# Optimization experiments

Measured on AMD Instinct MI355X. Metric: run time of the kernel, lower is better.

The kernel has to match this reference:

```python
import jax, jax.numpy as jnp
import numpy as np

B, T, NHANDS, DKP = 8, 1024, 2, 128
DM, H, DH, DFF, V, M, L = 1024, 16, 64, 4096, 2000, 256, 2
KEPS = 1e-4  # performer feature-map epsilon


def _orth_proj(key, m, d):
    # Gaussian orthogonal random features (FAVOR+), rows rescaled to chi norms
    n_blocks = int(np.ceil(m / d))
    blocks = []
    for i in range(n_blocks):
        q, _ = jnp.linalg.qr(jax.random.normal(jax.random.fold_in(key, i), (d, d)))
        blocks.append(q.T)
    mat = jnp.concatenate(blocks, 0)[:m]
    mult = jnp.linalg.norm(jax.random.normal(jax.random.fold_in(key, 10 ** 6), (m, d)), axis=1)
    return (mat * mult[:, None]).astype(jnp.float32)


def setup_inputs() -> dict:
    key = jax.random.key(0)
    ks = iter(jax.random.split(key, 64))
    w = lambda shape, s=0.02: (jax.random.normal(next(ks), shape) * s).astype(jnp.float32)
    z = lambda *shape: jnp.zeros(shape, jnp.float32)
    o = lambda *shape: jnp.ones(shape, jnp.float32)
    return {
        'x': jax.random.normal(next(ks), (B, T, NHANDS, DKP), dtype=jnp.float32),
        'Win': w((NHANDS * DKP, DM)), 'b_in': z(DM),
        'pe': jax.random.normal(next(ks), (5000, DM), dtype=jnp.float32),
        'ln1_g': o(L, DM), 'ln1_b': z(L, DM),
        'Wq': w((L, DM, DM)), 'bq': z(L, DM),
        'Wk': w((L, DM, DM)), 'bk': z(L, DM),
        'Wv': w((L, DM, DM)), 'bv': z(L, DM),
        'Wo': w((L, DM, DM)), 'bo': z(L, DM),
        'ln2_g': o(L, DM), 'ln2_b': z(L, DM),
        'W1': w((L, DM, DFF)), 'b1': z(L, DFF),
        'W2': w((L, DFF, DM)), 'b2': z(L, DM),
        'Wc': w((DM, V)), 'bc': z(V),
        'Wconv': w((64, DM, 3)), 'bconv': z(64),
        'Waux': w((64, V + 1)), 'baux': z(V + 1),
        'proj': _orth_proj(next(ks), M, DH),
    }


def _ln(x, g, b):
    mu = jnp.mean(x, -1, keepdims=True)
    var = jnp.mean((x - mu) ** 2, -1, keepdims=True)
    return (x - mu) / jnp.sqrt(var + 1e-5) * g + b


def _feats(data, proj, is_query):
    # FAVOR+ softmax kernel features, data: (B,H,T,DH) -> (B,H,T,M)
    dn = DH ** -0.25
    ratio = M ** -0.5
    dd = jnp.einsum('bhnd,md->bhnm', data, proj) * dn
    diag = jnp.sum(data ** 2, -1, keepdims=True) * 0.5 * dn * dn
    if is_query:
        stab = jnp.max(dd, -1, keepdims=True)
    else:
        stab = jnp.max(dd, (-1, -2), keepdims=True)
    return ratio * (jnp.exp(dd - diag - jax.lax.stop_gradient(stab)) + KEPS)


def reference(x, Win, b_in, pe, ln1_g, ln1_b, Wq, bq, Wk, bk, Wv, bv, Wo, bo,
              ln2_g, ln2_b, W1, b1, W2, b2, Wc, bc, Wconv, bconv, Waux, baux, proj):
    h = x.reshape(B, T, NHANDS * DKP) @ Win + b_in
    h = h + pe[:T][None]

    def layer(h, i):
        y = _ln(h, ln1_g[i], ln1_b[i])
        q = (y @ Wq[i] + bq[i]).reshape(B, T, H, DH).transpose(0, 2, 1, 3)
        k = (y @ Wk[i] + bk[i]).reshape(B, T, H, DH).transpose(0, 2, 1, 3)
        v = (y @ Wv[i] + bv[i]).reshape(B, T, H, DH).transpose(0, 2, 1, 3)
        qp = _feats(q, proj, True)   # (B,H,T,M)
        kp = _feats(k, proj, False)
        dinv = 1.0 / jnp.einsum('bhnm,bhm->bhn', qp, kp.sum(2))
        ctx = jnp.einsum('bhnm,bhnd->bhmd', kp, v)          # (B,H,M,DH)
        o = jnp.einsum('bhnm,bhmd->bhnd', qp, ctx) * dinv[..., None]
        o = o.transpose(0, 2, 1, 3).reshape(B, T, DM) @ Wo[i] + bo[i]
        h = h + o
        y = _ln(h, ln2_g[i], ln2_b[i])
        ff = jax.nn.gelu(y @ W1[i] + b1[i], approximate=False) @ W2[i] + b2[i]
        return h + ff

    h = layer(h, 0)
    xa = h.transpose(0, 2, 1)  # (B, DM, T)
    xa = jax.lax.conv_general_dilated(xa, Wconv, (1,), 'SAME',
                                      dimension_numbers=('NCH', 'OIH', 'NCH'))
    xa = xa + bconv[None, :, None]
    aux = xa.transpose(0, 2, 1) @ Waux + baux  # (B, T, V+1)
    h = layer(h, 1)
    gloss = h @ Wc + bc  # (B, T, V)
    return (gloss, aux)
```

## Files before the change

kernel.cpp:

```cpp
#include <hip/hip_runtime.h>
#include <hip/hip_bf16.h>

typedef __attribute__((ext_vector_type(4))) float f32x4;
typedef __attribute__((ext_vector_type(8))) unsigned short u16x8;
typedef __attribute__((ext_vector_type(4))) unsigned short u16x4;
typedef __bf16 bf16x8 __attribute__((ext_vector_type(8)));

#define DEVFN static __device__ __forceinline__

constexpr int CB = 8, CT = 1024, CDM = 1024, CH = 16, CDH = 64, CDFF = 4096, CV = 2000, CM = 256;
constexpr int CNT = CB * CT;
constexpr int CQKV = 3072;
constexpr float CDN = 0.35355339059327373f;
constexpr float CRATIO = 0.0625f;
constexpr float CKEPS = 1e-4f;

DEVFN unsigned short f2bu(float x) {
  __hip_bfloat16 h = __float2bfloat16(x);
  return __builtin_bit_cast(unsigned short, h);
}
DEVFN float b2f(unsigned short u) {
  __hip_bfloat16 h = __builtin_bit_cast(__hip_bfloat16, u);
  return __bfloat162float(h);
}
DEVFN float wredsum(float s) {
#pragma unroll
  for (int ofs = 32; ofs; ofs >>= 1) s += __shfl_xor(s, ofs, 64);
  return s;
}
DEVFN float wredmax(float s) {
#pragma unroll
  for (int ofs = 32; ofs; ofs >>= 1) s = fmaxf(s, __shfl_xor(s, ofs, 64));
  return s;
}
DEVFN void gl_lds16(const void* g, void* l) {
  __builtin_amdgcn_global_load_lds(
      (const __attribute__((address_space(1))) unsigned int*)g,
      (__attribute__((address_space(3))) unsigned int*)l, 16, 0, 0);
}
DEVFN f32x4 mfma16(u16x8 a, u16x8 b, f32x4 c) {
  return __builtin_amdgcn_mfma_f32_16x16x32_bf16(
      __builtin_bit_cast(bf16x8, a), __builtin_bit_cast(bf16x8, b), c, 0, 0, 0);
}
DEVFN u16x8 lds_rd128(unsigned addr) {
  u16x8 r;
  asm volatile("ds_read_b128 %0, %1" : "=v"(r) : "v"(addr));
  return r;
}
DEVFN unsigned lds_addr(const void* p) {
  return (unsigned)(unsigned long)(const __attribute__((address_space(3))) char*)p;
}

#define EPI_BIAS 1
#define EPI_ACCUM 2
#define EPI_GELU 4
#define EPI_OUTBF 8
#define EPI_RSCALE 16
#define EPI_PE 32
#define EPI_DUP 64

template <int EPI>
__global__ __launch_bounds__(512, 4) void gemm128_k(
    const unsigned short* __restrict__ A, const unsigned short* __restrict__ Bt,
    const float* __restrict__ bias, void* __restrict__ C, void* __restrict__ aux,
    int Mr, int Nr, int Kr, int lda, int ldb, int ldc) {
  __shared__ unsigned short smA[2][128 * 64];
  __shared__ unsigned short smB[2][128 * 64];

  int tid = threadIdx.x, wv = tid >> 6, ll = tid & 63;
  int wm = wv >> 2, wn = wv & 3;
  int m0 = blockIdx.x * 128, n0 = blockIdx.y * 128;
  int fr = ll & 15, f16 = ll >> 4, fk = f16 * 8;

  const char* Ab = (const char*)A;
  const char* Bb = (const char*)Bt;

  unsigned int offA[2], offB[2];
#pragma unroll
  for (int ro = 0; ro < 2; ro++) {
    int L = (ro * 512 + tid) * 16;
    int P = L ^ (((L >> 9) & 1) << 5);
    int kh = P >> 13, rem = P & 8191;
    int r = rem >> 6, cb = rem & 63;
    long rowA = min(m0 + r, Mr - 1);
    offA[ro] = (unsigned)((rowA * lda + kh * 32) * 2 + cb);
    long rowB = min(n0 + r, Nr - 1);
    offB[ro] = (unsigned)((rowB * ldb + kh * 32) * 2 + cb);
  }
  unsigned aAb = lds_addr(&smA[0][0]), aBb = lds_addr(&smB[0][0]);
  unsigned offArd[4], offBrd[2];
#pragma unroll
  for (int i = 0; i < 4; i++) {
    int r = wm * 64 + i * 16 + fr;
    offArd[i] = aAb + (unsigned)(r * 64 + 2 * (fk ^ (((r >> 3) & 1) << 4)));
  }
#pragma unroll
  for (int j = 0; j < 2; j++) {
    int r = wn * 32 + j * 16 + fr;
    offBrd[j] = aBb + (unsigned)(r * 64 + 2 * (fk ^ (((r >> 3) & 1) << 4)));
  }

  f32x4 acc[4][2] = {};
  int NT = Kr / 64;

#define STGALL(PB, KBN)                                                      \
  {                                                                          \
    _Pragma("unroll") for (int ro = 0; ro < 2; ro++)                         \
        gl_lds16(Ab + offA[ro] + (KBN), &smA[PB][(ro * 512 + wv * 64) * 8]); \
    _Pragma("unroll") for (int ro = 0; ro < 2; ro++)                         \
        gl_lds16(Bb + offB[ro] + (KBN), &smB[PB][(ro * 512 + wv * 64) * 8]); \
  }
#define TILE(PB, KBN)                                                        \
  {                                                                          \
    __builtin_amdgcn_s_barrier();                                            \
    __builtin_amdgcn_sched_barrier(0);                                       \
    STGALL((PB) ^ 1, KBN);                                                   \
    asm volatile("s_waitcnt vmcnt(4)" ::: "memory");                         \
    __builtin_amdgcn_sched_barrier(0);                                       \
    __builtin_amdgcn_s_barrier();                                            \
    __builtin_amdgcn_sched_barrier(0);                                       \
    u16x8 a0[4], b0[2], a1[4], b1[2];                                        \
    _Pragma("unroll") for (int i = 0; i < 4; i++)                            \
        a0[i] = lds_rd128(offArd[i] + (PB)*16384);                           \
    _Pragma("unroll") for (int j = 0; j < 2; j++)                            \
        b0[j] = lds_rd128(offBrd[j] + (PB)*16384);                           \
    _Pragma("unroll") for (int i = 0; i < 4; i++)                            \
        a1[i] = lds_rd128(offArd[i] + (PB)*16384 + 8192);                    \
    _Pragma("unroll") for (int j = 0; j < 2; j++)                            \
        b1[j] = lds_rd128(offBrd[j] + (PB)*16384 + 8192);                    \
    asm volatile("s_waitcnt lgkmcnt(6)" ::: "memory");                       \
    __builtin_amdgcn_sched_barrier(0);                                       \
    __builtin_amdgcn_s_setprio(1);                                           \
    _Pragma("unroll") for (int i = 0; i < 4; i++) {                          \
      acc[i][0] = mfma16(a0[i], b0[0], acc[i][0]);                           \
      acc[i][1] = mfma16(a0[i], b0[1], acc[i][1]);                           \
    }                                                                        \
    __builtin_amdgcn_s_setprio(0);                                           \
    asm volatile("s_waitcnt lgkmcnt(0)" ::: "memory");                       \
    __builtin_amdgcn_sched_barrier(0);                                       \
    __builtin_amdgcn_s_setprio(1);                                           \
    _Pragma("unroll") for (int i = 0; i < 4; i++) {                          \
      acc[i][0] = mfma16(a1[i], b1[0], acc[i][0]);                           \
      acc[i][1] = mfma16(a1[i], b1[1], acc[i][1]);                           \
    }                                                                        \
    __builtin_amdgcn_s_setprio(0);                                           \
  }

  STGALL(0, 0);
  for (int t = 0; t < NT; t += 2) {
    long kb1 = (long)(t + 1) * 128;
    long kb2 = (long)min(t + 2, NT - 1) * 128;
    TILE(0, kb1);
    TILE(1, kb2);
  }
  asm volatile("s_waitcnt vmcnt(0)" ::: "memory");
  __builtin_amdgcn_sched_barrier(0);
#undef TILE
#undef STGALL

#pragma unroll
  for (int i = 0; i < 4; i++) {
#pragma unroll
    for (int j = 0; j < 2; j++) {
#pragma unroll
      for (int e = 0; e < 4; e++) {
        int gr = m0 + wm * 64 + i * 16 + f16 * 4 + e;
        int gc = n0 + wn * 32 + j * 16 + fr;
        if (gr < Mr && gc < Nr) {
          float v = acc[i][j][e];
          if (EPI & EPI_BIAS) v += bias[gc];
          if (EPI & EPI_GELU) v = 0.5f * v * (1.0f + erff(v * 0.70710678118f));
          if (EPI & EPI_PE) v += ((const float*)aux)[((long)(gr & 1023) << 10) + gc];
          long idx = (long)gr * ldc + gc;
          if (EPI & EPI_ACCUM) v += ((float*)C)[idx];
          if (EPI & EPI_OUTBF) ((unsigned short*)C)[idx] = f2bu(v);
          else ((float*)C)[idx] = v;
          if (EPI & EPI_DUP) ((unsigned short*)aux)[idx] = f2bu(v);
        }
      }
    }
  }
}

template <int EPI, int MB, int NB>
__global__ __launch_bounds__(256) void gemm_k(
    const unsigned short* __restrict__ Aall, const unsigned short* __restrict__ Btall,
    const float* __restrict__ bias, void* __restrict__ Call, const float* __restrict__ rsall,
    int Mr, int Nr, int Kr, int lda, int ldb, int ldc, int bdiv,
    long As1, long As2, long Bs1, long Bs2, long Cs1, long Cs2, long Rs1, long Rs2) {
  __shared__ unsigned short smA[MB * 32];
  __shared__ unsigned short smB[NB * 32];
  constexpr int WRN = (MB == 128 && NB == 128) ? 2 : (MB == 128 ? 4 : 1);
  constexpr int WCN = 4 / WRN;
  constexpr int MT = MB / WRN, NTW = NB / WCN;
  constexpr int AF = MT / 16, BF = NTW / 16;
  int bz = blockIdx.z;
  const unsigned short* A = Aall + (long)(bz / bdiv) * As1 + (long)(bz % bdiv) * As2;
  const unsigned short* Bt = Btall + (long)(bz / bdiv) * Bs1 + (long)(bz % bdiv) * Bs2;
  long coff = (long)(bz / bdiv) * Cs1 + (long)(bz % bdiv) * Cs2;
  const float* rs = nullptr;
  if (EPI & EPI_RSCALE) rs = rsall + (long)(bz / bdiv) * Rs1 + (long)(bz % bdiv) * Rs2;

  int tid = threadIdx.x, wv = tid >> 6, ll = tid & 63;
  int m0 = blockIdx.x * MB, n0 = blockIdx.y * NB;
  int sr = tid >> 2, sc = (tid & 3) * 8;
  long ar0 = min(m0 + sr, Mr - 1);
  long ar1 = (MB == 128) ? min(m0 + sr + 64, (long)Mr - 1) : 0;
  long br0 = min(n0 + sr, Nr - 1);
  long br1 = (NB == 128) ? min(n0 + sr + 64, (long)Nr - 1) : 0;
  unsigned short* lA0 = &smA[(wv * 16) * 32];
  unsigned short* lA1 = &smA[(64 + wv * 16) * 32];
  unsigned short* lB0 = &smB[(wv * 16) * 32];
  unsigned short* lB1 = &smB[(64 + wv * 16) * 32];

  f32x4 acc[AF][BF] = {};
  int wr = (WRN == 1) ? 0 : ((WRN == 2) ? (wv >> 1) * MT : wv * MT);
  int wc = (WCN == 1) ? 0 : ((WCN == 2) ? (wv & 1) * NTW : wv * NTW);
  int fr = ll & 15, fk = (ll >> 4) * 8;

  for (int k0 = 0; k0 < Kr; k0 += 32) {
    __syncthreads();
    gl_lds16(A + ar0 * lda + k0 + sc, lA0);
    if (MB == 128) gl_lds16(A + ar1 * lda + k0 + sc, lA1);
    gl_lds16(Bt + br0 * ldb + k0 + sc, lB0);
    if (NB == 128) gl_lds16(Bt + br1 * ldb + k0 + sc, lB1);
    __syncthreads();
    u16x8 af[AF], bfr[BF];
#pragma unroll
    for (int i = 0; i < AF; i++) af[i] = *(const u16x8*)&smA[(wr + i * 16 + fr) * 32 + fk];
#pragma unroll
    for (int j = 0; j < BF; j++) bfr[j] = *(const u16x8*)&smB[(wc + j * 16 + fr) * 32 + fk];
#pragma unroll
    for (int i = 0; i < AF; i++)
#pragma unroll
      for (int j = 0; j < BF; j++) acc[i][j] = mfma16(af[i], bfr[j], acc[i][j]);
  }

#pragma unroll
  for (int i = 0; i < AF; i++) {
#pragma unroll
    for (int j = 0; j < BF; j++) {
#pragma unroll
      for (int e = 0; e < 4; e++) {
        int gr = m0 + wr + i * 16 + (ll >> 4) * 4 + e;
        int gc = n0 + wc + j * 16 + (ll & 15);
        if (gr < Mr && gc < Nr) {
          float v = acc[i][j][e];
          if (EPI & EPI_BIAS) v += bias[gc];
          if (EPI & EPI_GELU) v = 0.5f * v * (1.0f + erff(v * 0.70710678118f));
          if (EPI & EPI_RSCALE) v *= rs[gr];
          long idx = coff + (long)gr * ldc + gc;
          if (EPI & EPI_ACCUM) v += ((float*)Call)[idx];
          if (EPI & EPI_OUTBF) ((unsigned short*)Call)[idx] = f2bu(v);
          else ((float*)Call)[idx] = v;
        }
      }
    }
  }
}

DEVFN void feat_dd(const unsigned short* __restrict__ src, const unsigned short* __restrict__ projc,
                   unsigned short* ldsq, unsigned short* ldsp, int b, int t0, int hh,
                   f32x4 acc[16]) {
  int tid = threadIdx.x, wv = tid >> 6, ll = tid & 63;
#pragma unroll
  for (int p = 0; p < 2; p++) {
    int r = p * 64 + (tid >> 3), c8 = (tid & 7) * 8;
    *(u16x8*)&ldsq[r * 72 + c8] =
        *(const u16x8*)&src[((long)b * CT + t0 + r) * CQKV + hh * CDH + c8];
  }
#pragma unroll
  for (int p = 0; p < 4; p++) {
    int r = p * 64 + (tid >> 3), c8 = (tid & 7) * 8;
    *(u16x8*)&ldsp[r * 72 + c8] = *(const u16x8*)&projc[r * 64 + c8];
  }
  __syncthreads();
  int fr = ll & 15, fk = (ll >> 4) * 8;
#pragma unroll
  for (int ks = 0; ks < 2; ks++) {
    u16x8 af = *(const u16x8*)&ldsq[(wv * 16 + fr) * 72 + ks * 32 + fk];
#pragma unroll
    for (int j = 0; j < 16; j++) {
      u16x8 bf = *(const u16x8*)&ldsp[(j * 16 + fr) * 72 + ks * 32 + fk];
      acc[j] = mfma16(af, bf, acc[j]);
    }
  }
}

__global__ __launch_bounds__(512, 4) void kstab_f(const unsigned short* __restrict__ kb,
                                                  const unsigned short* __restrict__ projc,
                                                  float* __restrict__ part) {
  extern __shared__ char dynsm[];
  unsigned short* ldsq = (unsigned short*)dynsm;
  unsigned short* ldsp = (unsigned short*)(dynsm + 18432);
  __shared__ float smx[8];
  int bh = blockIdx.x >> 3, chunk = blockIdx.x & 7;
  int b = bh >> 4, hh = bh & 15;
  f32x4 acc[16] = {};
  feat_dd(kb, projc, ldsq, ldsp, b, chunk * 128, hh, acc);
  float mx = -3.4e38f;
#pragma unroll
  for (int j = 0; j < 16; j++)
#pragma unroll
    for (int e = 0; e < 4; e++) mx = fmaxf(mx, acc[j][e]);
  mx = wredmax(mx);
  int wv = threadIdx.x >> 6;
  if ((threadIdx.x & 63) == 0) smx[wv] = mx;
  __syncthreads();
  if (threadIdx.x == 0) {
    float m2 = smx[0];
#pragma unroll
    for (int i = 1; i < 8; i++) m2 = fmaxf(m2, smx[i]);
    part[blockIdx.x] = m2;
  }
}

__global__ __launch_bounds__(512, 4) void featk_f(const unsigned short* __restrict__ kb,
                                                  const unsigned short* __restrict__ projc,
                                                  const float* __restrict__ part,
                                                  unsigned short* __restrict__ kpt,
                                                  float* __restrict__ kspart) {
  extern __shared__ char dynsm[];
  unsigned short* ldsq = (unsigned short*)dynsm;
  unsigned short* ldsp = (unsigned short*)(dynsm + 18432);
  unsigned short* ldso = (unsigned short*)dynsm;
  int tid = threadIdx.x, wv = tid >> 6, ll = tid & 63;
  int bh = blockIdx.x >> 3, chunk = blockIdx.x & 7;
  int b = bh >> 4, hh = bh & 15;
  float st = part[bh * 8];
#pragma unroll
  for (int i = 1; i < 8; i++) st = fmaxf(st, part[bh * 8 + i]);
  f32x4 acc[16] = {};
  feat_dd(kb, projc, ldsq, ldsp, b, chunk * 128, hh, acc);
  int fr = ll & 15, g = ll >> 4;
  float diag[4];
#pragma unroll
  for (int e = 0; e < 4; e++) {
    int row = wv * 16 + g * 4 + e;
    u16x4 kv = *(const u16x4*)&ldsq[row * 72 + fr * 4];
    float s = 0;
#pragma unroll
    for (int z = 0; z < 4; z++) { float f = b2f(kv[z]); s += f * f; }
#pragma unroll
    for (int o = 1; o < 16; o <<= 1) s += __shfl_xor(s, o, 64);
    diag[e] = s * (0.5f * CDN * CDN);
  }
  __syncthreads();
#pragma unroll
  for (int j = 0; j < 16; j++)
#pragma unroll
    for (int e = 0; e < 4; e++) {
      float v = CRATIO * (expf(acc[j][e] - diag[e] - st) + CKEPS);
      ldso[(j * 16 + fr) * 136 + wv * 16 + g * 4 + e] = f2bu(v);
    }
  __syncthreads();
  int m = tid >> 1, seg = (tid & 1) * 64;
  long base = ((long)bh * CM + m) * CT + chunk * 128;
  float ks = 0;
#pragma unroll
  for (int z = 0; z < 8; z++) {
    u16x8 v8 = *(u16x8*)&ldso[m * 136 + seg + z * 8];
    *(u16x8*)&kpt[base + seg + z * 8] = v8;
#pragma unroll
    for (int w = 0; w < 8; w++) ks += b2f(v8[w]);
  }
  ks += __shfl_xor(ks, 1, 64);
  if ((tid & 1) == 0) kspart[((long)bh * 8 + chunk) * CM + m] = ks;
}

__global__ __launch_bounds__(512, 4) void featq_f(const unsigned short* __restrict__ qb,
                                                  const unsigned short* __restrict__ projc,
                                                  const float* __restrict__ kspart,
                                                  unsigned short* __restrict__ qp,
                                                  float* __restrict__ dinv) {
  extern __shared__ char dynsm[];
  unsigned short* ldsq = (unsigned short*)dynsm;
  unsigned short* ldsp = (unsigned short*)(dynsm + 18432);
  unsigned short* ldso = (unsigned short*)dynsm;
  float* ldks = (float*)(dynsm + 67584);
  int tid = threadIdx.x, wv = tid >> 6, ll = tid & 63;
  int bh = blockIdx.x >> 3, chunk = blockIdx.x & 7;
  int b = bh >> 4, hh = bh & 15;
  int t0 = chunk * 128;
  if (tid < 256) {
    float s = 0;
#pragma unroll
    for (int c = 0; c < 8; c++) s += kspart[((long)bh * 8 + c) * CM + tid];
    ldks[tid] = s;
  }
  f32x4 acc[16] = {};
  feat_dd(qb, projc, ldsq, ldsp, b, t0, hh, acc);
  int fr = ll & 15, g = ll >> 4;
  float rmax[4], diag[4];
#pragma unroll
  for (int e = 0; e < 4; e++) {
    float mx = acc[0][e];
#pragma unroll
    for (int j = 1; j < 16; j++) mx = fmaxf(mx, acc[j][e]);
#pragma unroll
    for (int o = 1; o < 16; o <<= 1) mx = fmaxf(mx, __shfl_xor(mx, o, 64));
    rmax[e] = mx;
    int row = wv * 16 + g * 4 + e;
    u16x4 qv = *(const u16x4*)&ldsq[row * 72 + fr * 4];
    float s = 0;
#pragma unroll
    for (int z = 0; z < 4; z++) { float f = b2f(qv[z]); s += f * f; }
#pragma unroll
    for (int o = 1; o < 16; o <<= 1) s += __shfl_xor(s, o, 64);
    diag[e] = s * (0.5f * CDN * CDN);
  }
  __syncthreads();
#pragma unroll
  for (int j = 0; j < 16; j++)
#pragma unroll
    for (int e = 0; e < 4; e++) {
      float v = CRATIO * (expf(acc[j][e] - diag[e] - rmax[e]) + CKEPS);
      ldso[(wv * 16 + g * 4 + e) * 264 + j * 16 + fr] = f2bu(v);
    }
  __syncthreads();
  int row = tid >> 2, seg = (tid & 3) * 64;
  long base = ((long)bh * CT + t0) * CM;
  float dot = 0;
#pragma unroll
  for (int z = 0; z < 8; z++) {
    u16x8 v8 = *(u16x8*)&ldso[row * 264 + seg + z * 8];
    *(u16x8*)&qp[base + (long)row * CM + seg + z * 8] = v8;
#pragma unroll
    for (int w = 0; w < 8; w++) dot += b2f(v8[w]) * ldks[seg + z * 8 + w];
  }
  dot += __shfl_xor(dot, 1, 64);
  dot += __shfl_xor(dot, 2, 64);
  if ((tid & 3) == 0) dinv[(long)bh * CT + t0 + row] = 1.0f / dot;
}

__global__ __launch_bounds__(256) void ln_k(const float* __restrict__ h,
                                            const float* __restrict__ g,
                                            const float* __restrict__ b,
                                            unsigned short* __restrict__ y) {
  int wv = threadIdx.x >> 6, ll = threadIdx.x & 63;
  long row = (long)blockIdx.x * 4 + wv;
  const float* hr = h + row * CDM;
  f32x4 x[4];
#pragma unroll
  for (int i = 0; i < 4; i++) x[i] = *(const f32x4*)&hr[ll * 16 + i * 4];
  float s = 0;
#pragma unroll
  for (int i = 0; i < 4; i++)
#pragma unroll
    for (int e = 0; e < 4; e++) s += x[i][e];
  float mu = wredsum(s) * (1.f / CDM);
  float v = 0;
#pragma unroll
  for (int i = 0; i < 4; i++)
#pragma unroll
    for (int e = 0; e < 4; e++) {
      float d = x[i][e] - mu;
      v += d * d;
    }
  float inv = rsqrtf(wredsum(v) * (1.f / CDM) + 1e-5f);
  unsigned short o[16];
#pragma unroll
  for (int i = 0; i < 4; i++)
#pragma unroll
    for (int e = 0; e < 4; e++) {
      int c = ll * 16 + i * 4 + e;
      o[i * 4 + e] = f2bu((x[i][e] - mu) * inv * g[c] + b[c]);
    }
  *(u16x8*)&y[row * CDM + ll * 16] = *(u16x8*)&o[0];
  *(u16x8*)&y[row * CDM + ll * 16 + 8] = *(u16x8*)&o[8];
}

__global__ __launch_bounds__(256) void trv_k(const unsigned short* __restrict__ vb,
                                             unsigned short* __restrict__ vt) {
  int bh = blockIdx.x >> 5;
  int t0 = (blockIdx.x & 31) * 32;
  int b = bh >> 4, hh = bh & 15;
  __shared__ unsigned short tile[32][64];
  int tr = threadIdx.x >> 3, dblk = (threadIdx.x & 7) * 8;
  *(u16x8*)&tile[tr][dblk] = *(const u16x8*)&vb[((long)b * CT + t0 + tr) * CQKV + hh * CDH + dblk];
  __syncthreads();
  int d = threadIdx.x >> 2, tz = (threadIdx.x & 3) * 8;
  unsigned short o[8];
#pragma unroll
  for (int e = 0; e < 8; e++) o[e] = tile[tz + e][d];
  *(u16x8*)&vt[((long)bh * CDH + d) * CT + t0 + tz] = *(u16x8*)&o[0];
}

__global__ __launch_bounds__(256) void f2b_k(const float* __restrict__ in,
                                             unsigned short* __restrict__ out, long n) {
  long i = ((long)blockIdx.x * 256 + threadIdx.x) * 4;
  if (i >= n) return;
  f32x4 v = *(const f32x4*)&in[i];
  unsigned short o[4];
#pragma unroll
  for (int e = 0; e < 4; e++) o[e] = f2bu(v[e]);
  *(u16x4*)&out[i] = *(u16x4*)&o[0];
}

__global__ __launch_bounds__(256) void tconvz_k(const float* __restrict__ in,
                                                unsigned short* __restrict__ out, int R, int C,
                                                long szs, long dzs) {
  const float* src = in + (long)blockIdx.z * szs;
  unsigned short* dst = out + (long)blockIdx.z * dzs;
  __shared__ float tile[32][33];
  int r0 = blockIdx.x * 32, c0 = blockIdx.y * 32;
  int tr = threadIdx.x >> 5, tc = threadIdx.x & 31;
#pragma unroll
  for (int p = 0; p < 4; p++) {
    int r = r0 + p * 8 + tr, c = c0 + tc;
    tile[p * 8 + tr][tc] = (r < R && c < C) ? src[(long)r * C + c] : 0.f;
  }
  __syncthreads();
#pragma unroll
  for (int p = 0; p < 4; p++) {
    int c = c0 + p * 8 + tr, r = r0 + tc;
    if (c < C && r < R) dst[(long)c * R + r] = f2bu(tile[tc][p * 8 + tr]);
  }
}

__global__ __launch_bounds__(256) void wconv_k(const float* __restrict__ W,
                                               unsigned short* __restrict__ out) {
  int idx = blockIdx.x * 256 + threadIdx.x;
  int r = idx >> 16, rem = idx & 65535, oc = rem >> 10, ic = rem & 1023;
  out[idx] = f2bu(W[oc * 3072 + ic * 3 + r]);
}

__global__ __launch_bounds__(256) void convmix_k(const float* __restrict__ Y,
                                                 const float* __restrict__ bc,
                                                 float* __restrict__ xa) {
  long t = (long)blockIdx.x * 4 + (threadIdx.x >> 6);
  int oc = threadIdx.x & 63;
  int tb = (int)(t & 1023);
  float v = Y[t * 192 + 64 + oc] + bc[oc];
  if (tb != 0) v += Y[(t - 1) * 192 + oc];
  if (tb != 1023) v += Y[(t + 1) * 192 + 128 + oc];
  xa[t * 64 + oc] = v;
}

__global__ __launch_bounds__(256) void projc_k(const float* __restrict__ p,
                                               unsigned short* __restrict__ out) {
  int i = blockIdx.x * 256 + threadIdx.x;
  out[i] = f2bu(p[i] * CDN);
}

__global__ __launch_bounds__(256) void catb_k(const float* __restrict__ q,
                                              const float* __restrict__ k,
                                              const float* __restrict__ v,
                                              float* __restrict__ o) {
  int l = blockIdx.y;
  int i = blockIdx.x * 256 + threadIdx.x;
  float val = i < 1024 ? q[l * CDM + i] : (i < 2048 ? k[l * CDM + i - 1024] : v[l * CDM + i - 2048]);
  o[l * CQKV + i] = val;
}

#define LAUNCH_GEMM(EPI, MB, NB, A, Bt, bias, C, rsp, Mr, Nr, Kr, lda, ldb, ldc, nb, bdiv, As1, As2, Bs1, Bs2, Cs1, Cs2, Rs1, Rs2) \
  gemm_k<EPI, MB, NB><<<dim3(((Mr) + (MB)-1) / (MB), ((Nr) + (NB)-1) / (NB), (nb)), 256, 0, stream>>>( \
      (const unsigned short*)(A), (const unsigned short*)(Bt), (bias), (void*)(C), (rsp),        \
      (Mr), (Nr), (Kr), (lda), (ldb), (ldc), (bdiv), (long)(As1), (long)(As2), (long)(Bs1),      \
      (long)(Bs2), (long)(Cs1), (long)(Cs2), (long)(Rs1), (long)(Rs2))

#define LAUNCH_G1(EPI, A, Bt, bias, C, AUX, Mr, Nr, Kr, lda, ldb, ldc)                           \
  gemm128_k<EPI><<<dim3(((Mr) + 127) / 128, ((Nr) + 127) / 128), 512, 0, stream>>>(              \
      (const unsigned short*)(A), (const unsigned short*)(Bt), (bias), (void*)(C), (void*)(AUX), \
      (Mr), (Nr), (Kr), (lda), (ldb), (ldc))

extern "C" void kernel_launch(void* const* d_in, const int* in_sizes, int n_in,
                              void* d_out, int out_size, void* d_ws, size_t ws_size,
                              hipStream_t stream) {
  const float* x = (const float*)d_in[0];
  const float* Win = (const float*)d_in[1];
  const float* b_in = (const float*)d_in[2];
  const float* pe = (const float*)d_in[3];
  const float* ln1_g = (const float*)d_in[4];
  const float* ln1_b = (const float*)d_in[5];
  const float* Wq = (const float*)d_in[6];
  const float* bq = (const float*)d_in[7];
  const float* Wk = (const float*)d_in[8];
  const float* bk = (const float*)d_in[9];
  const float* Wv = (const float*)d_in[10];
  const float* bv = (const float*)d_in[11];
  const float* Wo = (const float*)d_in[12];
  const float* bo = (const float*)d_in[13];
  const float* ln2_g = (const float*)d_in[14];
  const float* ln2_b = (const float*)d_in[15];
  const float* W1 = (const float*)d_in[16];
  const float* b1 = (const float*)d_in[17];
  const float* W2 = (const float*)d_in[18];
  const float* b2 = (const float*)d_in[19];
  const float* Wc = (const float*)d_in[20];
  const float* bc = (const float*)d_in[21];
  const float* Wconv = (const float*)d_in[22];
  const float* bconv = (const float*)d_in[23];
  const float* Waux = (const float*)d_in[24];
  const float* baux = (const float*)d_in[25];
  const float* proj = (const float*)d_in[26];
  float* out = (float*)d_out;

  char* wsp = (char*)d_ws;
  size_t off = 0;
  auto take = [&](size_t bytes) {
    char* p = wsp + off;
    off = (off + bytes + 255) & ~(size_t)255;
    return p;
  };
  float* h_f = (float*)take(33554432);
  unsigned short* y_bf = (unsigned short*)take(16777216);
  unsigned short* qkv_bf = (unsigned short*)take(50331648);
  unsigned short* qp_bf = (unsigned short*)take(67108864);
  unsigned short* kpt_bf = (unsigned short*)take(67108864);
  unsigned short* ff_bf = (unsigned short*)take(67108864);
  unsigned short* ctx_bf = (unsigned short*)take(4194304);
  float* kspart_f = (float*)take(1048576);
  float* kstab_f_buf = (float*)take(4096);
  float* dinv_f = (float*)take(524288);
  float* xa_f = (float*)take(2097152);
  float* ycv_f = (float*)take(6291456);
  unsigned short* xabf = (unsigned short*)take(1048576);
  float* bqkv_f = (float*)take(24576);
  unsigned short* hbf = (unsigned short*)take(16777216);
  unsigned short* xbf = (unsigned short*)take(4194304);
  unsigned short* win_t = (unsigned short*)take(524288);
  unsigned short* wqkvo_t = (unsigned short*)take(16777216);
  unsigned short* w1_t = (unsigned short*)take(16777216);
  unsigned short* w2_t = (unsigned short*)take(16777216);
  unsigned short* wc_t = (unsigned short*)take(4096000);
  unsigned short* projc = (unsigned short*)take(32768);
  unsigned short* wconv_t = (unsigned short*)take(393216);
  unsigned short* waux_t = (unsigned short*)take(256128);
  unsigned short* vt_bf = y_bf;
  unsigned short* o_bf = y_bf;
  (void)in_sizes; (void)n_in; (void)out_size; (void)ws_size;

  f2b_k<<<2048, 256, 0, stream>>>(x, xbf, (long)CNT * 256);
  tconvz_k<<<dim3(8, 32, 1), 256, 0, stream>>>(Win, win_t, 256, 1024, 0, 0);
  tconvz_k<<<dim3(32, 32, 2), 256, 0, stream>>>(Wq, wqkvo_t + 0 * 1048576, 1024, 1024, 1048576, 4194304);
  tconvz_k<<<dim3(32, 32, 2), 256, 0, stream>>>(Wk, wqkvo_t + 1 * 1048576, 1024, 1024, 1048576, 4194304);
  tconvz_k<<<dim3(32, 32, 2), 256, 0, stream>>>(Wv, wqkvo_t + 2 * 1048576, 1024, 1024, 1048576, 4194304);
  tconvz_k<<<dim3(32, 32, 2), 256, 0, stream>>>(Wo, wqkvo_t + 3 * 1048576, 1024, 1024, 1048576, 4194304);
  tconvz_k<<<dim3(32, 128, 2), 256, 0, stream>>>(W1, w1_t, 1024, 4096, 4194304, 4194304);
  tconvz_k<<<dim3(128, 32, 2), 256, 0, stream>>>(W2, w2_t, 4096, 1024, 4194304, 4194304);
  tconvz_k<<<dim3(32, 63, 1), 256, 0, stream>>>(Wc, wc_t, 1024, 2000, 0, 0);
  tconvz_k<<<dim3(2, 63, 1), 256, 0, stream>>>(Waux, waux_t, 64, 2001, 0, 0);
  catb_k<<<dim3(12, 2), 256, 0, stream>>>(bq, bk, bv, bqkv_f);
  wconv_k<<<768, 256, 0, stream>>>(Wconv, wconv_t);
  projc_k<<<64, 256, 0, stream>>>(proj, projc);

  LAUNCH_G1(EPI_BIAS | EPI_PE, xbf, win_t, b_in, h_f, pe, CNT, CDM, 256, 256, 256, CDM);

  for (int l = 0; l < 2; l++) {
    const unsigned short* wqkv_t = wqkvo_t + (long)(l * 4) * 1048576;
    const unsigned short* wo_t = wqkvo_t + (long)(l * 4 + 3) * 1048576;

    ln_k<<<2048, 256, 0, stream>>>(h_f, ln1_g + l * CDM, ln1_b + l * CDM, y_bf);
    LAUNCH_G1(EPI_BIAS | EPI_OUTBF, y_bf, wqkv_t, bqkv_f + l * CQKV, qkv_bf, nullptr, CNT, CQKV, CDM, CDM, CDM, CQKV);

    kstab_f<<<1024, 512, 55296, stream>>>(qkv_bf + 1024, projc, kstab_f_buf);
    featk_f<<<1024, 512, 69632, stream>>>(qkv_bf + 1024, projc, kstab_f_buf, kpt_bf, kspart_f);
    featq_f<<<1024, 512, 68608, stream>>>(qkv_bf, projc, kspart_f, qp_bf, dinv_f);
    trv_k<<<4096, 256, 0, stream>>>(qkv_bf + 2048, vt_bf);
    LAUNCH_GEMM(EPI_OUTBF, 64, 128, vt_bf, kpt_bf, nullptr, ctx_bf, nullptr, CDH, CM, CT, CT, CT, CM, 128, CH,
                (long)CH * CDH * CT, (long)CDH * CT, (long)CH * CM * CT, (long)CM * CT,
                (long)CH * CDH * CM, (long)CDH * CM, 0, 0);
    LAUNCH_GEMM(EPI_RSCALE | EPI_OUTBF, 128, 64, qp_bf, ctx_bf, nullptr, o_bf, dinv_f, CT, CDH, CM, CM, CM, CDM, 128, CH,
                (long)CH * CT * CM, (long)CT * CM, (long)CH * CDH * CM, (long)CDH * CM,
                (long)CT * CDM, 64, (long)CH * CT, (long)CT);
    LAUNCH_G1(EPI_BIAS | EPI_ACCUM, o_bf, wo_t, bo + l * CDM, h_f, nullptr, CNT, CDM, CDM, CDM, CDM, CDM);

    ln_k<<<2048, 256, 0, stream>>>(h_f, ln2_g + l * CDM, ln2_b + l * CDM, y_bf);
    LAUNCH_G1(EPI_BIAS | EPI_GELU | EPI_OUTBF, y_bf, w1_t + (long)l * 4194304, b1 + l * CDFF, ff_bf, nullptr,
              CNT, CDFF, CDM, CDM, CDM, CDFF);
    LAUNCH_G1(EPI_BIAS | EPI_ACCUM | EPI_DUP, ff_bf, w2_t + (long)l * 4194304, b2 + l * CDM, h_f, hbf,
              CNT, CDM, CDFF, CDFF, CDFF, CDM);

    if (l == 0) {
      LAUNCH_GEMM(0, 128, 128, hbf, wconv_t, nullptr, ycv_f, nullptr, CNT, 192, CDM, CDM, CDM, 192, 1, 1, 0, 0, 0, 0, 0, 0, 0, 0);
      convmix_k<<<2048, 256, 0, stream>>>(ycv_f, bconv, xa_f);
      f2b_k<<<512, 256, 0, stream>>>(xa_f, xabf, (long)CNT * 64);
      LAUNCH_GEMM(EPI_BIAS, 128, 128, xabf, waux_t, baux, out + 16384000, nullptr, CNT, CV + 1, 64, 64, 64, CV + 1, 1, 1, 0, 0, 0, 0, 0, 0, 0, 0);
    }
  }

  LAUNCH_G1(EPI_BIAS, hbf, wc_t, bc, out, nullptr, CNT, CV, CDM, CDM, CDM, CV);
}
```

Baseline: 1.214 ms.

## Fuse query features with context matmul and fold conv bf16 cast into convmix

The query feature kernel now computes the normalizer and immediately multiplies the in-LDS query features by the per-head context via MFMA, writing the attention output directly. This removes the 64MB qp buffer round trip, the dinv buffer and a separate batched GEMM launch. The ctx GEMM is reordered to run before the fused kernel. Separately, convmix writes bf16 directly, dropping an f2b pass and an fp32 intermediate. The fused kernel reads ctx from global memory without LDS staging, which may cost some bandwidth.

```diff
diff --git a/kernel.cpp b/kernel.cpp
--- a/kernel.cpp
+++ b/kernel.cpp
@@ -55,7 +55,6 @@
 #define EPI_ACCUM 2
 #define EPI_GELU 4
 #define EPI_OUTBF 8
-#define EPI_RSCALE 16
 #define EPI_PE 32
 #define EPI_DUP 64
 
@@ -185,9 +184,9 @@
 template <int EPI, int MB, int NB>
 __global__ __launch_bounds__(256) void gemm_k(
     const unsigned short* __restrict__ Aall, const unsigned short* __restrict__ Btall,
-    const float* __restrict__ bias, void* __restrict__ Call, const float* __restrict__ rsall,
+    const float* __restrict__ bias, void* __restrict__ Call,
     int Mr, int Nr, int Kr, int lda, int ldb, int ldc, int bdiv,
-    long As1, long As2, long Bs1, long Bs2, long Cs1, long Cs2, long Rs1, long Rs2) {
+    long As1, long As2, long Bs1, long Bs2, long Cs1, long Cs2) {
   __shared__ unsigned short smA[MB * 32];
   __shared__ unsigned short smB[NB * 32];
   constexpr int WRN = (MB == 128 && NB == 128) ? 2 : (MB == 128 ? 4 : 1);
@@ -198,8 +197,6 @@
   const unsigned short* A = Aall + (long)(bz / bdiv) * As1 + (long)(bz % bdiv) * As2;
   const unsigned short* Bt = Btall + (long)(bz / bdiv) * Bs1 + (long)(bz % bdiv) * Bs2;
   long coff = (long)(bz / bdiv) * Cs1 + (long)(bz % bdiv) * Cs2;
-  const float* rs = nullptr;
-  if (EPI & EPI_RSCALE) rs = rsall + (long)(bz / bdiv) * Rs1 + (long)(bz % bdiv) * Rs2;
 
   int tid = threadIdx.x, wv = tid >> 6, ll = tid & 63;
   int m0 = blockIdx.x * MB, n0 = blockIdx.y * NB;
@@ -247,10 +244,7 @@
         if (gr < Mr && gc < Nr) {
           float v = acc[i][j][e];
           if (EPI & EPI_BIAS) v += bias[gc];
-          if (EPI & EPI_GELU) v = 0.5f * v * (1.0f + erff(v * 0.70710678118f));
-          if (EPI & EPI_RSCALE) v *= rs[gr];
           long idx = coff + (long)gr * ldc + gc;
-          if (EPI & EPI_ACCUM) v += ((float*)Call)[idx];
           if (EPI & EPI_OUTBF) ((unsigned short*)Call)[idx] = f2bu(v);
           else ((float*)Call)[idx] = v;
         }
@@ -368,16 +362,17 @@
   if ((tid & 1) == 0) kspart[((long)bh * 8 + chunk) * CM + m] = ks;
 }
 
-__global__ __launch_bounds__(512, 4) void featq_f(const unsigned short* __restrict__ qb,
-                                                  const unsigned short* __restrict__ projc,
-                                                  const float* __restrict__ kspart,
-                                                  unsigned short* __restrict__ qp,
-                                                  float* __restrict__ dinv) {
+__global__ __launch_bounds__(512, 4) void featqo_f(const unsigned short* __restrict__ qb,
+                                                   const unsigned short* __restrict__ projc,
+                                                   const float* __restrict__ kspart,
+                                                   const unsigned short* __restrict__ ctxall,
+                                                   unsigned short* __restrict__ obuf) {
   extern __shared__ char dynsm[];
   unsigned short* ldsq = (unsigned short*)dynsm;
   unsigned short* ldsp = (unsigned short*)(dynsm + 18432);
   unsigned short* ldso = (unsigned short*)dynsm;
   float* ldks = (float*)(dynsm + 67584);
+  float* ldinv = (float*)(dynsm + 68608);
   int tid = threadIdx.x, wv = tid >> 6, ll = tid & 63;
   int bh = blockIdx.x >> 3, chunk = blockIdx.x & 7;
   int b = bh >> 4, hh = bh & 15;
@@ -390,7 +385,7 @@
   }
   f32x4 acc[16] = {};
   feat_dd(qb, projc, ldsq, ldsp, b, t0, hh, acc);
-  int fr = ll & 15, g = ll >> 4;
+  int fr = ll & 15, g = ll >> 4, fk = g * 8;
   float rmax[4], diag[4];
 #pragma unroll
   for (int e = 0; e < 4; e++) {
@@ -418,19 +413,39 @@
       ldso[(wv * 16 + g * 4 + e) * 264 + j * 16 + fr] = f2bu(v);
     }
   __syncthreads();
-  int row = tid >> 2, seg = (tid & 3) * 64;
-  long base = ((long)bh * CT + t0) * CM;
-  float dot = 0;
-#pragma unroll
-  for (int z = 0; z < 8; z++) {
-    u16x8 v8 = *(u16x8*)&ldso[row * 264 + seg + z * 8];
-    *(u16x8*)&qp[base + (long)row * CM + seg + z * 8] = v8;
-#pragma unroll
-    for (int w = 0; w < 8; w++) dot += b2f(v8[w]) * ldks[seg + z * 8 + w];
-  }
-  dot += __shfl_xor(dot, 1, 64);
-  dot += __shfl_xor(dot, 2, 64);
-  if ((tid & 3) == 0) dinv[(long)bh * CT + t0 + row] = 1.0f / dot;
+  {
+    int row = tid >> 2, seg = (tid & 3) * 64;
+    float dot = 0;
+#pragma unroll
+    for (int z = 0; z < 8; z++) {
+      u16x8 v8 = *(u16x8*)&ldso[row * 264 + seg + z * 8];
+#pragma unroll
+      for (int w = 0; w < 8; w++) dot += b2f(v8[w]) * ldks[seg + z * 8 + w];
+    }
+    dot += __shfl_xor(dot, 1, 64);
+    dot += __shfl_xor(dot, 2, 64);
+    if ((tid & 3) == 0) ldinv[row] = 1.0f / dot;
+  }
+  const unsigned short* ctxb = ctxall + (long)bh * 16384;
+  f32x4 ao[4] = {};
+#pragma unroll
+  for (int ks = 0; ks < 8; ks++) {
+    u16x8 af = *(const u16x8*)&ldso[(wv * 16 + fr) * 264 + ks * 32 + fk];
+#pragma unroll
+    for (int j = 0; j < 4; j++) {
+      u16x8 bf = *(const u16x8*)&ctxb[(j * 16 + fr) * 256 + ks * 32 + fk];
+      ao[j] = mfma16(af, bf, ao[j]);
+    }
+  }
+  __syncthreads();
+#pragma unroll
+  for (int j = 0; j < 4; j++)
+#pragma unroll
+    for (int e = 0; e < 4; e++) {
+      int r = wv * 16 + g * 4 + e;
+      float v = ao[j][e] * ldinv[r];
+      obuf[((long)b * CT + t0 + r) * CDM + hh * CDH + j * 16 + fr] = f2bu(v);
+    }
 }
 
 __global__ __launch_bounds__(256) void ln_k(const float* __restrict__ h,
@@ -527,14 +542,14 @@
 
 __global__ __launch_bounds__(256) void convmix_k(const float* __restrict__ Y,
                                                  const float* __restrict__ bc,
-                                                 float* __restrict__ xa) {
+                                                 unsigned short* __restrict__ xab) {
   long t = (long)blockIdx.x * 4 + (threadIdx.x >> 6);
   int oc = threadIdx.x & 63;
   int tb = (int)(t & 1023);
   float v = Y[t * 192 + 64 + oc] + bc[oc];
   if (tb != 0) v += Y[(t - 1) * 192 + oc];
   if (tb != 1023) v += Y[(t + 1) * 192 + 128 + oc];
-  xa[t * 64 + oc] = v;
+  xab[t * 64 + oc] = f2bu(v);
 }
 
 __global__ __launch_bounds__(256) void projc_k(const float* __restrict__ p,
@@ -553,11 +568,11 @@
   o[l * CQKV + i] = val;
 }
 
-#define LAUNCH_GEMM(EPI, MB, NB, A, Bt, bias, C, rsp, Mr, Nr, Kr, lda, ldb, ldc, nb, bdiv, As1, As2, Bs1, Bs2, Cs1, Cs2, Rs1, Rs2) \
+#define LAUNCH_GEMM(EPI, MB, NB, A, Bt, bias, C, Mr, Nr, Kr, lda, ldb, ldc, nb, bdiv, As1, As2, Bs1, Bs2, Cs1, Cs2) \
   gemm_k<EPI, MB, NB><<<dim3(((Mr) + (MB)-1) / (MB), ((Nr) + (NB)-1) / (NB), (nb)), 256, 0, stream>>>( \
-      (const unsigned short*)(A), (const unsigned short*)(Bt), (bias), (void*)(C), (rsp),        \
+      (const unsigned short*)(A), (const unsigned short*)(Bt), (bias), (void*)(C),               \
       (Mr), (Nr), (Kr), (lda), (ldb), (ldc), (bdiv), (long)(As1), (long)(As2), (long)(Bs1),      \
-      (long)(Bs2), (long)(Cs1), (long)(Cs2), (long)(Rs1), (long)(Rs2))
+      (long)(Bs2), (long)(Cs1), (long)(Cs2))
 
 #define LAUNCH_G1(EPI, A, Bt, bias, C, AUX, Mr, Nr, Kr, lda, ldb, ldc)                           \
   gemm128_k<EPI><<<dim3(((Mr) + 127) / 128, ((Nr) + 127) / 128), 512, 0, stream>>>(              \
@@ -606,14 +621,11 @@
   float* h_f = (float*)take(33554432);
   unsigned short* y_bf = (unsigned short*)take(16777216);
   unsigned short* qkv_bf = (unsigned short*)take(50331648);
-  unsigned short* qp_bf = (unsigned short*)take(67108864);
   unsigned short* kpt_bf = (unsigned short*)take(67108864);
   unsigned short* ff_bf = (unsigned short*)take(67108864);
   unsigned short* ctx_bf = (unsigned short*)take(4194304);
   float* kspart_f = (float*)take(1048576);
   float* kstab_f_buf = (float*)take(4096);
-  float* dinv_f = (float*)take(524288);
-  float* xa_f = (float*)take(2097152);
   float* ycv_f = (float*)take(6291456);
   unsigned short* xabf = (unsigned short*)take(1048576);
   float* bqkv_f = (float*)take(24576);
@@ -656,14 +668,11 @@
 
     kstab_f<<<1024, 512, 55296, stream>>>(qkv_bf + 1024, projc, kstab_f_buf);
     featk_f<<<1024, 512, 69632, stream>>>(qkv_bf + 1024, projc, kstab_f_buf, kpt_bf, kspart_f);
-    featq_f<<<1024, 512, 68608, stream>>>(qkv_bf, projc, kspart_f, qp_bf, dinv_f);
     trv_k<<<4096, 256, 0, stream>>>(qkv_bf + 2048, vt_bf);
-    LAUNCH_GEMM(EPI_OUTBF, 64, 128, vt_bf, kpt_bf, nullptr, ctx_bf, nullptr, CDH, CM, CT, CT, CT, CM, 128, CH,
+    LAUNCH_GEMM(EPI_OUTBF, 64, 128, vt_bf, kpt_bf, nullptr, ctx_bf, CDH, CM, CT, CT, CT, CM, 128, CH,
                 (long)CH * CDH * CT, (long)CDH * CT, (long)CH * CM * CT, (long)CM * CT,
-                (long)CH * CDH * CM, (long)CDH * CM, 0, 0);
-    LAUNCH_GEMM(EPI_RSCALE | EPI_OUTBF, 128, 64, qp_bf, ctx_bf, nullptr, o_bf, dinv_f, CT, CDH, CM, CM, CM, CDM, 128, CH,
-                (long)CH * CT * CM, (long)CT * CM, (long)CH * CDH * CM, (long)CDH * CM,
-                (long)CT * CDM, 64, (long)CH * CT, (long)CT);
+                (long)CH * CDH * CM, (long)CDH * CM);
+    featqo_f<<<1024, 512, 69120, stream>>>(qkv_bf, projc, kspart_f, ctx_bf, o_bf);
     LAUNCH_G1(EPI_BIAS | EPI_ACCUM, o_bf, wo_t, bo + l * CDM, h_f, nullptr, CNT, CDM, CDM, CDM, CDM, CDM);
 
     ln_k<<<2048, 256, 0, stream>>>(h_f, ln2_g + l * CDM, ln2_b + l * CDM, y_bf);
@@ -673,10 +682,9 @@
               CNT, CDM, CDFF, CDFF, CDFF, CDM);
 
     if (l == 0) {
-      LAUNCH_GEMM(0, 128, 128, hbf, wconv_t, nullptr, ycv_f, nullptr, CNT, 192, CDM, CDM, CDM, 192, 1, 1, 0, 0, 0, 0, 0, 0, 0, 0);
-      convmix_k<<<2048, 256, 0, stream>>>(ycv_f, bconv, xa_f);
-      f2b_k<<<512, 256, 0, stream>>>(xa_f, xabf, (long)CNT * 64);
-      LAUNCH_GEMM(EPI_BIAS, 128, 128, xabf, waux_t, baux, out + 16384000, nullptr, CNT, CV + 1, 64, 64, 64, CV + 1, 1, 1, 0, 0, 0, 0, 0, 0, 0, 0);
+      LAUNCH_GEMM(0, 128, 128, hbf, wconv_t, nullptr, ycv_f, CNT, 192, CDM, CDM, CDM, 192, 1, 1, 0, 0, 0, 0, 0, 0);
+      convmix_k<<<2048, 256, 0, stream>>>(ycv_f, bconv, xabf);
+      LAUNCH_GEMM(EPI_BIAS, 128, 128, xabf, waux_t, baux, out + 16384000, CNT, CV + 1, 64, 64, 64, CV + 1, 1, 1, 0, 0, 0, 0, 0, 0);
     }
   }
 
```

Result: faster. 1.167 ms (-3.8%).
